# Kernel optimization log

Measured on AMD Instinct MI355X. Metric: run time of the kernel, lower is better.

## Reference

```python
import jax, jax.numpy as jnp
import numpy as np

B, N, D, K = 4, 16384, 16, 64  # batch, pixels, input_dim, output_dim
SCALE_INIT = 1.0 / (5.0 * 16)  # Constant(1/(5*scale_dim)) initializer


def setup_inputs() -> dict:
    key = jax.random.key(0)
    k1, k2 = jax.random.split(key)
    x = jax.random.normal(k1, (B, N, D), dtype=jnp.float32)
    centers = jax.random.uniform(k2, (K, D), dtype=jnp.float32)  # RandomUniform(0,1)
    scaling = jnp.full((1, 1, D, 1), SCALE_INIT, dtype=jnp.float32)
    return {"x": x, "centers": centers, "scaling": scaling}


def reference(x, centers, scaling):
    # scaling broadcasts per input feature: extract (D,) vector
    s = scaling[0, 0, :, 0]                      # (D,)
    Hx = x * s                                   # (B,N,D) == H[...,0] in original
    Cs = s[:, None] * centers.T                  # (D,K) scaled centers
    diff = Hx[..., None] - Cs                    # (B,N,D,K) broadcast pairwise diff
    O = jnp.sum(diff * diff, axis=-2)            # (B,N,K) squared distances
    return (O, Hx)
```

## Files before the change

### kernel.cpp

```cpp
#include <hip/hip_runtime.h>


constexpr int D = 16;
constexpr int K = 64;
constexpr int ROWS_PER_BLOCK = 32;
constexpr int BLOCK = 256;

__global__ __launch_bounds__(BLOCK) void rbf_kernel(
    const float* __restrict__ x,
    const float* __restrict__ centers,
    const float* __restrict__ scaling,
    float* __restrict__ O,
    float* __restrict__ Hx,
    int nRows)
{
    const int tid  = threadIdx.x;
    const int lane = tid & 63;
    const int rgrp = tid >> 6;

    __shared__ float hx_sh[ROWS_PER_BLOCK * D];

    const int blockRow0 = blockIdx.x * ROWS_PER_BLOCK;

    {
        const float2* xsrc = reinterpret_cast<const float2*>(x + (size_t)blockRow0 * D);
        const float2* s2p  = reinterpret_cast<const float2*>(scaling);
        float2 v  = xsrc[tid];
        float2 s2 = s2p[tid & 7];
        float2 h;
        h.x = v.x * s2.x;
        h.y = v.y * s2.y;
        reinterpret_cast<float2*>(hx_sh)[tid] = h;
        reinterpret_cast<float2*>(Hx + (size_t)blockRow0 * D)[tid] = h;
    }

    float cs[D];
    {
        const float4* c4 = reinterpret_cast<const float4*>(centers + lane * D);
        const float4* s4 = reinterpret_cast<const float4*>(scaling);
        #pragma unroll
        for (int q = 0; q < 4; ++q) {
            float4 cv = c4[q];
            float4 sv = s4[q];
            cs[4 * q + 0] = cv.x * sv.x;
            cs[4 * q + 1] = cv.y * sv.y;
            cs[4 * q + 2] = cv.z * sv.z;
            cs[4 * q + 3] = cv.w * sv.w;
        }
    }

    __syncthreads();

    const float4* hx4 = reinterpret_cast<const float4*>(hx_sh);
    #pragma unroll
    for (int r = 0; r < ROWS_PER_BLOCK / 4; ++r) {
        const int localRow = r * 4 + rgrp;
        const int row = blockRow0 + localRow;
        if (row >= nRows) break;

        float4 h0 = hx4[localRow * 4 + 0];
        float4 h1 = hx4[localRow * 4 + 1];
        float4 h2 = hx4[localRow * 4 + 2];
        float4 h3 = hx4[localRow * 4 + 3];

        float acc = 0.f;
        float d0;
        d0 = h0.x - cs[0];  acc = fmaf(d0, d0, acc);
        d0 = h0.y - cs[1];  acc = fmaf(d0, d0, acc);
        d0 = h0.z - cs[2];  acc = fmaf(d0, d0, acc);
        d0 = h0.w - cs[3];  acc = fmaf(d0, d0, acc);
        d0 = h1.x - cs[4];  acc = fmaf(d0, d0, acc);
        d0 = h1.y - cs[5];  acc = fmaf(d0, d0, acc);
        d0 = h1.z - cs[6];  acc = fmaf(d0, d0, acc);
        d0 = h1.w - cs[7];  acc = fmaf(d0, d0, acc);
        d0 = h2.x - cs[8];  acc = fmaf(d0, d0, acc);
        d0 = h2.y - cs[9];  acc = fmaf(d0, d0, acc);
        d0 = h2.z - cs[10]; acc = fmaf(d0, d0, acc);
        d0 = h2.w - cs[11]; acc = fmaf(d0, d0, acc);
        d0 = h3.x - cs[12]; acc = fmaf(d0, d0, acc);
        d0 = h3.y - cs[13]; acc = fmaf(d0, d0, acc);
        d0 = h3.z - cs[14]; acc = fmaf(d0, d0, acc);
        d0 = h3.w - cs[15]; acc = fmaf(d0, d0, acc);

        O[(size_t)row * K + lane] = acc;
    }
}

extern "C" void kernel_launch(void* const* d_in, const int* in_sizes, int n_in,
                              void* d_out, int out_size, void* d_ws, size_t ws_size,
                              hipStream_t stream) {
    const float* x       = (const float*)d_in[0];
    const float* centers = (const float*)d_in[1];
    const float* scaling = (const float*)d_in[2];

    const int nRows = in_sizes[0] / D;
    float* O  = (float*)d_out;
    float* Hx = (float*)d_out + (size_t)nRows * K;

    const int grid = (nRows + ROWS_PER_BLOCK - 1) / ROWS_PER_BLOCK;
    rbf_kernel<<<grid, BLOCK, 0, stream>>>(x, centers, scaling, O, Hx, nRows);
}
```

Baseline: 12.83 us.

## Double rows per block, use float4 x loads, give each wave contiguous rows

Each block now handles 64 rows instead of 32, so it launches half as many blocks and amortizes the per-block center scaling. The x input is loaded as float4, the scaling vector is loaded once and reused for both Hx and the centers, and the Hx store is moved to after the compute loop. Each wave now processes 16 contiguous rows rather than interleaved rows, and the row bounds check is removed, so nRows must be a multiple of 64.

```diff
diff --git a/kernel.cpp b/kernel.cpp
--- a/kernel.cpp
+++ b/kernel.cpp
@@ -3,7 +3,7 @@
 
 constexpr int D = 16;
 constexpr int K = 64;
-constexpr int ROWS_PER_BLOCK = 32;
+constexpr int ROWS_PER_BLOCK = 64;
 constexpr int BLOCK = 256;
 
 __global__ __launch_bounds__(BLOCK) void rbf_kernel(
@@ -16,36 +16,39 @@
 {
     const int tid  = threadIdx.x;
     const int lane = tid & 63;
-    const int rgrp = tid >> 6;
+    const int wid  = tid >> 6;
 
     __shared__ float hx_sh[ROWS_PER_BLOCK * D];
 
     const int blockRow0 = blockIdx.x * ROWS_PER_BLOCK;
 
+    const float4* s4p = reinterpret_cast<const float4*>(scaling);
+    float4 sv[4];
+    #pragma unroll
+    for (int q = 0; q < 4; ++q) sv[q] = s4p[q];
+
+    float4 h;
     {
-        const float2* xsrc = reinterpret_cast<const float2*>(x + (size_t)blockRow0 * D);
-        const float2* s2p  = reinterpret_cast<const float2*>(scaling);
-        float2 v  = xsrc[tid];
-        float2 s2 = s2p[tid & 7];
-        float2 h;
-        h.x = v.x * s2.x;
-        h.y = v.y * s2.y;
-        reinterpret_cast<float2*>(hx_sh)[tid] = h;
-        reinterpret_cast<float2*>(Hx + (size_t)blockRow0 * D)[tid] = h;
+        const float4* x4 = reinterpret_cast<const float4*>(x + (size_t)blockRow0 * D);
+        float4 v = x4[tid];
+        float4 sq = sv[tid & 3];
+        h.x = v.x * sq.x;
+        h.y = v.y * sq.y;
+        h.z = v.z * sq.z;
+        h.w = v.w * sq.w;
+        reinterpret_cast<float4*>(hx_sh)[tid] = h;
     }
 
     float cs[D];
     {
         const float4* c4 = reinterpret_cast<const float4*>(centers + lane * D);
-        const float4* s4 = reinterpret_cast<const float4*>(scaling);
         #pragma unroll
         for (int q = 0; q < 4; ++q) {
             float4 cv = c4[q];
-            float4 sv = s4[q];
-            cs[4 * q + 0] = cv.x * sv.x;
-            cs[4 * q + 1] = cv.y * sv.y;
-            cs[4 * q + 2] = cv.z * sv.z;
-            cs[4 * q + 3] = cv.w * sv.w;
+            cs[4 * q + 0] = cv.x * sv[q].x;
+            cs[4 * q + 1] = cv.y * sv[q].y;
+            cs[4 * q + 2] = cv.z * sv[q].z;
+            cs[4 * q + 3] = cv.w * sv[q].w;
         }
     }
 
@@ -53,10 +56,8 @@
 
     const float4* hx4 = reinterpret_cast<const float4*>(hx_sh);
     #pragma unroll
-    for (int r = 0; r < ROWS_PER_BLOCK / 4; ++r) {
-        const int localRow = r * 4 + rgrp;
-        const int row = blockRow0 + localRow;
-        if (row >= nRows) break;
+    for (int r = 0; r < 16; ++r) {
+        const int localRow = wid * 16 + r;
 
         float4 h0 = hx4[localRow * 4 + 0];
         float4 h1 = hx4[localRow * 4 + 1];
@@ -82,8 +83,10 @@
         d0 = h3.z - cs[14]; acc = fmaf(d0, d0, acc);
         d0 = h3.w - cs[15]; acc = fmaf(d0, d0, acc);
 
-        O[(size_t)row * K + lane] = acc;
+        O[(size_t)(blockRow0 + localRow) * K + lane] = acc;
     }
+
+    reinterpret_cast<float4*>(Hx + (size_t)blockRow0 * D)[tid] = h;
 }
 
 extern "C" void kernel_launch(void* const* d_in, const int* in_sizes, int n_in,
```

Result: slower. 26.17 us (+104.0%).
